# Performance work log

Measured on AMD Instinct MI355X. Metric: run time of the kernel, lower is better.

The kernel has to match this reference:

```python
import jax, jax.numpy as jnp
import numpy as np

N = 16384          # num nodes
D_IN, D_HID, D_OUT = 512, 256, 64
S = 4096           # sampled nodes per layer


def setup_inputs() -> dict:
    key = jax.random.key(0)
    ks = jax.random.split(key, 8)
    X = jax.random.normal(ks[0], (N, D_IN), dtype=jnp.float32)
    A_hat = jax.random.uniform(ks[1], (N, N), dtype=jnp.float32)
    W1 = jax.random.normal(ks[2], (D_IN, D_HID), dtype=jnp.float32) * 0.05
    b1 = jax.random.normal(ks[3], (D_HID,), dtype=jnp.float32) * 0.05
    W2 = jax.random.normal(ks[4], (D_HID, D_OUT), dtype=jnp.float32) * 0.05
    b2 = jax.random.normal(ks[5], (D_OUT,), dtype=jnp.float32) * 0.05
    # unique sampled node ids per layer (avoids nondeterministic duplicate scatter)
    sampled_l0 = jax.random.permutation(ks[6], N)[:S].astype(jnp.int32)
    sampled_l1 = jax.random.permutation(ks[7], N)[:S].astype(jnp.int32)
    return {"X": X, "A_hat": A_hat, "W1": W1, "b1": b1, "W2": W2, "b2": b2,
            "sampled_l0": sampled_l0, "sampled_l1": sampled_l1}


def reference(X, A_hat, W1, b1, W2, b2, sampled_l0, sampled_l1):
    n = X.shape[0]
    s0 = sampled_l0.shape[0]
    s1 = sampled_l1.shape[0]

    # ---- layer 0: sampled = l0, next_sampled = l1 ----
    H_l = jax.nn.relu(X[sampled_l0] @ W1 + b1)                 # [S, D_HID]
    # weights[i,j] = A_hat[next[i], sampled[j]] * N / S  (sampling_probs=None path)
    w0 = A_hat[sampled_l1][:, sampled_l0] * (n / s0)           # [S, S]
    agg0 = w0 @ H_l                                            # [S, D_HID]
    H = jnp.zeros((n, W1.shape[1]), dtype=X.dtype).at[sampled_l1].set(agg0)
    H = jax.nn.relu(H)                                         # inter-layer relu

    # ---- layer 1 (last): sampled = l1, next_sampled = arange(N) ----
    H_l2 = jax.nn.relu(H[sampled_l1] @ W2 + b2)                # [S, D_OUT]
    w1 = A_hat[:, sampled_l1] * (n / s1)                       # [N, S]
    out = w1 @ H_l2                                            # [N, D_OUT]; scatter to arange(N) == identity
    return out
```

## Files before the change

kernel.cpp:

```cpp
#include <hip/hip_runtime.h>
#include <hip/hip_bf16.h>
#include <stdint.h>

typedef __attribute__((ext_vector_type(8))) short short8;
typedef __attribute__((ext_vector_type(4))) float f32x4;

#define N_NODES 16384
#define D_IN    512
#define D_HID   256
#define D_OUT   64
#define S_SAMP  4096

__device__ __forceinline__ unsigned short f2bf(float f) {
  __hip_bfloat16 h = __float2bfloat16(f);
  union { __hip_bfloat16 h; unsigned short u; } cv; cv.h = h; return cv.u;
}

template<int BM, int BN, int BK, bool RELU_A>
__global__ __launch_bounds__(256)
void gemm_tn(const float* __restrict__ A, int lda,
             const int* __restrict__ arow,
             const unsigned short* __restrict__ Bt, int ldb,
             float* __restrict__ C, int ldc,
             int K, int kChunks, float scale)
{
  static_assert(BM == 64 && BK == 64 && (BN == 64 || BN == 256), "tile");
  const int mt  = blockIdx.x / kChunks;
  const int kc  = blockIdx.x % kChunks;
  const int kLen = K / kChunks;
  const int k0   = kc * kLen;
  const int tid  = threadIdx.x;
  const int lane = tid & 63;
  const int wid  = tid >> 6;
  const int l16  = lane & 15;
  const int lg   = lane >> 4;

  __shared__ unsigned short As[BM * BK];
  __shared__ unsigned short Bs[BN * BK];

  constexpr int WN  = (BN == 256) ? 4 : 2;
  constexpr int WM  = 4 / WN;
  constexpr int WTM = BM / WM;
  constexpr int WTN = BN / WN;
  constexpr int MF  = WTM / 16;
  constexpr int NF  = WTN / 16;
  const int wrow = wid / WN;
  const int wcol = wid % WN;

  f32x4 acc[MF][NF] = {};

  const int am   = tid >> 2;
  const int aseg = tid & 3;
  const int arowIdx = mt * BM + am;
  const size_t rowg = arow ? (size_t)arow[arowIdx] : (size_t)arowIdx;
  const float* aBase = A + rowg * (size_t)lda + k0 + aseg * 16;

  constexpr int SLABS = BN / 8;
  constexpr int SLABW = SLABS / 4;
  const int brow = lane >> 3;
  const int bcol = 8 * ((lane & 7) ^ brow);
  const unsigned short* bSrcLane = Bt + (size_t)brow * ldb + k0 + bcol;

  for (int ks = 0; ks < kLen; ks += BK) {
    __syncthreads();
    #pragma unroll
    for (int i = 0; i < SLABW; ++i) {
      const int s = wid * SLABW + i;
      __builtin_amdgcn_global_load_lds(
          (const __attribute__((address_space(1))) uint32_t*)(bSrcLane + (size_t)s * 8 * ldb + ks),
          (__attribute__((address_space(3))) uint32_t*)(&Bs[s * 512]),
          16, 0, 0);
    }
    {
      const float* ap = aBase + ks;
      f32x4 v0 = *(const f32x4*)(ap + 0);
      f32x4 v1 = *(const f32x4*)(ap + 4);
      f32x4 v2 = *(const f32x4*)(ap + 8);
      f32x4 v3 = *(const f32x4*)(ap + 12);
      if (RELU_A) {
        #pragma unroll
        for (int j = 0; j < 4; ++j) {
          v0[j] = fmaxf(v0[j], 0.f); v1[j] = fmaxf(v1[j], 0.f);
          v2[j] = fmaxf(v2[j], 0.f); v3[j] = fmaxf(v3[j], 0.f);
        }
      }
      short8 s0, s1;
      s0[0]=f2bf(v0[0]); s0[1]=f2bf(v0[1]); s0[2]=f2bf(v0[2]); s0[3]=f2bf(v0[3]);
      s0[4]=f2bf(v1[0]); s0[5]=f2bf(v1[1]); s0[6]=f2bf(v1[2]); s0[7]=f2bf(v1[3]);
      s1[0]=f2bf(v2[0]); s1[1]=f2bf(v2[1]); s1[2]=f2bf(v2[2]); s1[3]=f2bf(v2[3]);
      s1[4]=f2bf(v3[0]); s1[5]=f2bf(v3[1]); s1[6]=f2bf(v3[2]); s1[7]=f2bf(v3[3]);
      const int g0 = (aseg * 2)     ^ (am & 7);
      const int g1 = (aseg * 2 + 1) ^ (am & 7);
      *(short8*)&As[am * BK + g0 * 8] = s0;
      *(short8*)&As[am * BK + g1 * 8] = s1;
    }
    __syncthreads();
    #pragma unroll
    for (int kk = 0; kk < BK / 32; ++kk) {
      const int gk = kk * 4 + lg;
      short8 af[MF], bfr[NF];
      #pragma unroll
      for (int fm = 0; fm < MF; ++fm) {
        const int m = wrow * WTM + fm * 16 + l16;
        af[fm] = *(const short8*)&As[m * BK + ((gk ^ (m & 7)) * 8)];
      }
      #pragma unroll
      for (int fn = 0; fn < NF; ++fn) {
        const int n = wcol * WTN + fn * 16 + l16;
        bfr[fn] = *(const short8*)&Bs[n * BK + ((gk ^ (n & 7)) * 8)];
      }
      #pragma unroll
      for (int fm = 0; fm < MF; ++fm)
        #pragma unroll
        for (int fn = 0; fn < NF; ++fn)
          acc[fm][fn] = __builtin_amdgcn_mfma_f32_16x16x32_bf16(
              af[fm], bfr[fn], acc[fm][fn], 0, 0, 0);
    }
  }
  #pragma unroll
  for (int fm = 0; fm < MF; ++fm)
    #pragma unroll
    for (int fn = 0; fn < NF; ++fn)
      #pragma unroll
      for (int j = 0; j < 4; ++j) {
        const int r = mt * BM + wrow * WTM + fm * 16 + lg * 4 + j;
        const int c = wcol * WTN + fn * 16 + l16;
        atomicAdd(&C[(size_t)r * ldc + c], scale * acc[fm][fn][j]);
      }
}

__global__ void conv_w_t(const float* __restrict__ W1, const float* __restrict__ W2,
                         unsigned short* __restrict__ W1t, unsigned short* __restrict__ W2t) {
  const int idx = blockIdx.x * 256 + threadIdx.x;
  if (idx < D_IN * D_HID) {
    const int j = idx / D_IN, i = idx % D_IN;
    W1t[idx] = f2bf(W1[(size_t)i * D_HID + j]);
  }
  if (idx < D_HID * D_OUT) {
    const int j = idx / D_HID, i = idx % D_HID;
    W2t[idx] = f2bf(W2[(size_t)i * D_OUT + j]);
  }
}

__global__ void ep_scatter_t(const float* __restrict__ G, const float* __restrict__ bias,
                             const int* __restrict__ rows, unsigned short* __restrict__ BextT,
                             int ncol, int total) {
  const int idx = blockIdx.x * 256 + threadIdx.x;
  if (idx >= total) return;
  const int c = idx / S_SAMP;
  const int r = idx & (S_SAMP - 1);
  float v = G[(size_t)r * ncol + c] + bias[c];
  v = v > 0.f ? v : 0.f;
  BextT[(size_t)c * N_NODES + rows[r]] = f2bf(v);
}

extern "C" void kernel_launch(void* const* d_in, const int* in_sizes, int n_in,
                              void* d_out, int out_size, void* d_ws, size_t ws_size,
                              hipStream_t stream) {
  const float* X     = (const float*)d_in[0];
  const float* A_hat = (const float*)d_in[1];
  const float* W1    = (const float*)d_in[2];
  const float* b1    = (const float*)d_in[3];
  const float* W2    = (const float*)d_in[4];
  const float* b2    = (const float*)d_in[5];
  const int*   l0    = (const int*)d_in[6];
  const int*   l1    = (const int*)d_in[7];
  float* out = (float*)d_out;

  if (ws_size < (size_t)(20u << 20)) return;
  char* ws = (char*)d_ws;
  unsigned short* HextT = (unsigned short*)(ws);
  unsigned short* PextT = (unsigned short*)(ws + (8  << 20));
  float* G1 = (float*)(ws + (10 << 20));
  float* G2 = (float*)(ws + (14 << 20));
  float* G3 = (float*)(ws + (18 << 20));
  unsigned short* W1t = (unsigned short*)(ws + (19 << 20));
  unsigned short* W2t = (unsigned short*)(ws + (19 << 20) + (256 << 10));

  hipMemsetAsync(ws,  0, (size_t)(19u << 20), stream);
  hipMemsetAsync(out, 0, (size_t)N_NODES * D_OUT * 4, stream);

  conv_w_t<<<512, 256, 0, stream>>>(W1, W2, W1t, W2t);

  gemm_tn<64, 256, 64, false><<<(S_SAMP / 64) * 4, 256, 0, stream>>>(
      X, D_IN, l0, W1t, D_IN, G1, D_HID, D_IN, 4, 1.0f);
  ep_scatter_t<<<(S_SAMP * D_HID + 255) / 256, 256, 0, stream>>>(
      G1, b1, l0, HextT, D_HID, S_SAMP * D_HID);

  gemm_tn<64, 256, 64, false><<<(S_SAMP / 64) * 8, 256, 0, stream>>>(
      A_hat, N_NODES, l1, HextT, N_NODES, G2, D_HID, N_NODES, 8, 4.0f);

  gemm_tn<64, 64, 64, true><<<(S_SAMP / 64) * 4, 256, 0, stream>>>(
      G2, D_HID, nullptr, W2t, D_HID, G3, D_OUT, D_HID, 4, 1.0f);
  ep_scatter_t<<<(S_SAMP * D_OUT + 255) / 256, 256, 0, stream>>>(
      G3, b2, l1, PextT, D_OUT, S_SAMP * D_OUT);

  gemm_tn<64, 64, 64, false><<<(N_NODES / 64) * 8, 256, 0, stream>>>(
      A_hat, N_NODES, nullptr, PextT, N_NODES, out, D_OUT, N_NODES, 8, 4.0f);
}
```

Measured before the change: 370.3 us.

## Double-buffer LDS tiles in GEMM and retune BK and split-K counts

The GEMM kernel now keeps two LDS buffers. While the current tile is computed, the next A tile is prefetched into registers and the next B tile is issued with global_load_lds, which is meant to hide global load latency behind MFMA work. BK is made configurable (32 or 64) with matching swizzle parameters. The launches are retuned: the first two GEMMs use BK=32, the A_hat×H GEMM uses 16 K-chunks, and the final N×S GEMM uses 4. The extra buffer doubles LDS use and raises register pressure, which may reduce occupancy, and more K-chunks means more atomic traffic.

```diff
diff --git a/kernel.cpp b/kernel.cpp
--- a/kernel.cpp
+++ b/kernel.cpp
@@ -24,19 +24,27 @@
              float* __restrict__ C, int ldc,
              int K, int kChunks, float scale)
 {
-  static_assert(BM == 64 && BK == 64 && (BN == 64 || BN == 256), "tile");
+  static_assert(BM == 64 && (BK == 32 || BK == 64) && (BN == 64 || BN == 256), "tile");
+  constexpr int CH    = BK / 8;
+  constexpr int RPS   = 512 / BK;
+  constexpr int SLABS = BN / RPS;
+  constexpr int SLABW = SLABS / 4;
+  constexpr int AV    = BK / 16;
+  constexpr int AC    = BK / 32;
+
   const int mt  = blockIdx.x / kChunks;
   const int kc  = blockIdx.x % kChunks;
   const int kLen = K / kChunks;
   const int k0   = kc * kLen;
+  const int nt   = kLen / BK;
   const int tid  = threadIdx.x;
   const int lane = tid & 63;
   const int wid  = tid >> 6;
   const int l16  = lane & 15;
   const int lg   = lane >> 4;
 
-  __shared__ unsigned short As[BM * BK];
-  __shared__ unsigned short Bs[BN * BK];
+  __shared__ unsigned short As[2][BM * BK];
+  __shared__ unsigned short Bs[2][BN * BK];
 
   constexpr int WN  = (BN == 256) ? 4 : 2;
   constexpr int WM  = 4 / WN;
@@ -53,48 +61,47 @@
   const int aseg = tid & 3;
   const int arowIdx = mt * BM + am;
   const size_t rowg = arow ? (size_t)arow[arowIdx] : (size_t)arowIdx;
-  const float* aBase = A + rowg * (size_t)lda + k0 + aseg * 16;
-
-  constexpr int SLABS = BN / 8;
-  constexpr int SLABW = SLABS / 4;
-  const int brow = lane >> 3;
-  const int bcol = 8 * ((lane & 7) ^ brow);
-  const unsigned short* bSrcLane = Bt + (size_t)brow * ldb + k0 + bcol;
-
-  for (int ks = 0; ks < kLen; ks += BK) {
-    __syncthreads();
+  const float* aBase = A + rowg * (size_t)lda + k0 + aseg * (BK / 4);
+
+  const int brow = lane / CH;
+  const int bcol = 8 * ((lane % CH) ^ (brow & (CH - 1)));
+  const unsigned short* bSrc = Bt + (size_t)brow * ldb + k0 + bcol;
+
+  f32x4 av[AV];
+
+  auto loadA = [&](int ks) {
+    #pragma unroll
+    for (int i = 0; i < AV; ++i) av[i] = *(const f32x4*)(aBase + ks + 4 * i);
+  };
+  auto writeA = [&](int buf) {
+    if (RELU_A) {
+      #pragma unroll
+      for (int i = 0; i < AV; ++i)
+        #pragma unroll
+        for (int j = 0; j < 4; ++j) av[i][j] = fmaxf(av[i][j], 0.f);
+    }
+    #pragma unroll
+    for (int c = 0; c < AC; ++c) {
+      short8 s;
+      s[0]=f2bf(av[2*c][0]);   s[1]=f2bf(av[2*c][1]);
+      s[2]=f2bf(av[2*c][2]);   s[3]=f2bf(av[2*c][3]);
+      s[4]=f2bf(av[2*c+1][0]); s[5]=f2bf(av[2*c+1][1]);
+      s[6]=f2bf(av[2*c+1][2]); s[7]=f2bf(av[2*c+1][3]);
+      const int g = (aseg * AC + c) ^ (am & (CH - 1));
+      *(short8*)&As[buf][am * BK + g * 8] = s;
+    }
+  };
+  auto issueB = [&](int buf, int ks) {
     #pragma unroll
     for (int i = 0; i < SLABW; ++i) {
       const int s = wid * SLABW + i;
       __builtin_amdgcn_global_load_lds(
-          (const __attribute__((address_space(1))) uint32_t*)(bSrcLane + (size_t)s * 8 * ldb + ks),
-          (__attribute__((address_space(3))) uint32_t*)(&Bs[s * 512]),
+          (const __attribute__((address_space(1))) uint32_t*)(bSrc + (size_t)s * RPS * ldb + ks),
+          (__attribute__((address_space(3))) uint32_t*)(&Bs[buf][s * 512]),
           16, 0, 0);
     }
-    {
-      const float* ap = aBase + ks;
-      f32x4 v0 = *(const f32x4*)(ap + 0);
-      f32x4 v1 = *(const f32x4*)(ap + 4);
-      f32x4 v2 = *(const f32x4*)(ap + 8);
-      f32x4 v3 = *(const f32x4*)(ap + 12);
-      if (RELU_A) {
-        #pragma unroll
-        for (int j = 0; j < 4; ++j) {
-          v0[j] = fmaxf(v0[j], 0.f); v1[j] = fmaxf(v1[j], 0.f);
-          v2[j] = fmaxf(v2[j], 0.f); v3[j] = fmaxf(v3[j], 0.f);
-        }
-      }
-      short8 s0, s1;
-      s0[0]=f2bf(v0[0]); s0[1]=f2bf(v0[1]); s0[2]=f2bf(v0[2]); s0[3]=f2bf(v0[3]);
-      s0[4]=f2bf(v1[0]); s0[5]=f2bf(v1[1]); s0[6]=f2bf(v1[2]); s0[7]=f2bf(v1[3]);
-      s1[0]=f2bf(v2[0]); s1[1]=f2bf(v2[1]); s1[2]=f2bf(v2[2]); s1[3]=f2bf(v2[3]);
-      s1[4]=f2bf(v3[0]); s1[5]=f2bf(v3[1]); s1[6]=f2bf(v3[2]); s1[7]=f2bf(v3[3]);
-      const int g0 = (aseg * 2)     ^ (am & 7);
-      const int g1 = (aseg * 2 + 1) ^ (am & 7);
-      *(short8*)&As[am * BK + g0 * 8] = s0;
-      *(short8*)&As[am * BK + g1 * 8] = s1;
-    }
-    __syncthreads();
+  };
+  auto compute = [&](int buf) {
     #pragma unroll
     for (int kk = 0; kk < BK / 32; ++kk) {
       const int gk = kk * 4 + lg;
@@ -102,12 +109,12 @@
       #pragma unroll
       for (int fm = 0; fm < MF; ++fm) {
         const int m = wrow * WTM + fm * 16 + l16;
-        af[fm] = *(const short8*)&As[m * BK + ((gk ^ (m & 7)) * 8)];
+        af[fm] = *(const short8*)&As[buf][m * BK + ((gk ^ (m & (CH - 1))) * 8)];
       }
       #pragma unroll
       for (int fn = 0; fn < NF; ++fn) {
         const int n = wcol * WTN + fn * 16 + l16;
-        bfr[fn] = *(const short8*)&Bs[n * BK + ((gk ^ (n & 7)) * 8)];
+        bfr[fn] = *(const short8*)&Bs[buf][n * BK + ((gk ^ (n & (CH - 1))) * 8)];
       }
       #pragma unroll
       for (int fm = 0; fm < MF; ++fm)
@@ -116,7 +123,26 @@
           acc[fm][fn] = __builtin_amdgcn_mfma_f32_16x16x32_bf16(
               af[fm], bfr[fn], acc[fm][fn], 0, 0, 0);
     }
+  };
+
+  loadA(0);
+  issueB(0, 0);
+  writeA(0);
+  __syncthreads();
+
+  int cur = 0;
+  for (int t = 0; t < nt; ++t) {
+    const bool more = (t + 1 < nt);
+    if (more) {
+      loadA((t + 1) * BK);
+      issueB(cur ^ 1, (t + 1) * BK);
+    }
+    compute(cur);
+    if (more) writeA(cur ^ 1);
+    __syncthreads();
+    cur ^= 1;
   }
+
   #pragma unroll
   for (int fm = 0; fm < MF; ++fm)
     #pragma unroll
@@ -182,19 +208,19 @@
 
   conv_w_t<<<512, 256, 0, stream>>>(W1, W2, W1t, W2t);
 
-  gemm_tn<64, 256, 64, false><<<(S_SAMP / 64) * 4, 256, 0, stream>>>(
+  gemm_tn<64, 256, 32, false><<<(S_SAMP / 64) * 4, 256, 0, stream>>>(
       X, D_IN, l0, W1t, D_IN, G1, D_HID, D_IN, 4, 1.0f);
   ep_scatter_t<<<(S_SAMP * D_HID + 255) / 256, 256, 0, stream>>>(
       G1, b1, l0, HextT, D_HID, S_SAMP * D_HID);
 
-  gemm_tn<64, 256, 64, false><<<(S_SAMP / 64) * 8, 256, 0, stream>>>(
-      A_hat, N_NODES, l1, HextT, N_NODES, G2, D_HID, N_NODES, 8, 4.0f);
+  gemm_tn<64, 256, 32, false><<<(S_SAMP / 64) * 16, 256, 0, stream>>>(
+      A_hat, N_NODES, l1, HextT, N_NODES, G2, D_HID, N_NODES, 16, 4.0f);
 
   gemm_tn<64, 64, 64, true><<<(S_SAMP / 64) * 4, 256, 0, stream>>>(
       G2, D_HID, nullptr, W2t, D_HID, G3, D_OUT, D_HID, 4, 1.0f);
   ep_scatter_t<<<(S_SAMP * D_OUT + 255) / 256, 256, 0, stream>>>(
       G3, b2, l1, PextT, D_OUT, S_SAMP * D_OUT);
 
-  gemm_tn<64, 64, 64, false><<<(N_NODES / 64) * 8, 256, 0, stream>>>(
-      A_hat, N_NODES, nullptr, PextT, N_NODES, out, D_OUT, N_NODES, 8, 4.0f);
-}
+  gemm_tn<64, 64, 64, false><<<(N_NODES / 64) * 4, 256, 0, stream>>>(
+      A_hat, N_NODES, nullptr, PextT, N_NODES, out, D_OUT, N_NODES, 4, 4.0f);
+}
```

Result: slower. 423.9 us (+14.5%).

## Add double-buffered streaming GEMM for final aggregation and split K further

Applied to the files above, without the earlier changes.

Adds a gemm_stream kernel for the large A_hat @ P aggregation. It loads A rows straight into registers in MFMA fragment layout, skipping the LDS staging of A, and double-buffers the B tiles via global_load_lds with explicit waitcnt and barriers, so the next tile's loads overlap the current MFMAs. The first two GEMMs also double their K-split counts for more blocks, which adds atomic traffic on the output. The B-load indexing in gemm_tn is generalised, and a min-waves launch bound targets higher occupancy.

```diff
diff --git a/kernel.cpp b/kernel.cpp
--- a/kernel.cpp
+++ b/kernel.cpp
@@ -25,6 +25,11 @@
              int K, int kChunks, float scale)
 {
   static_assert(BM == 64 && BK == 64 && (BN == 64 || BN == 256), "tile");
+  constexpr int CH    = BK / 8;
+  constexpr int RPS   = 512 / BK;
+  constexpr int SLABS = BN / RPS;
+  constexpr int SLABW = SLABS / 4;
+
   const int mt  = blockIdx.x / kChunks;
   const int kc  = blockIdx.x % kChunks;
   const int kLen = K / kChunks;
@@ -55,11 +60,9 @@
   const size_t rowg = arow ? (size_t)arow[arowIdx] : (size_t)arowIdx;
   const float* aBase = A + rowg * (size_t)lda + k0 + aseg * 16;
 
-  constexpr int SLABS = BN / 8;
-  constexpr int SLABW = SLABS / 4;
-  const int brow = lane >> 3;
-  const int bcol = 8 * ((lane & 7) ^ brow);
-  const unsigned short* bSrcLane = Bt + (size_t)brow * ldb + k0 + bcol;
+  const int brow = lane / CH;
+  const int bcol = 8 * ((lane % CH) ^ (brow & (CH - 1)));
+  const unsigned short* bSrc = Bt + (size_t)brow * ldb + k0 + bcol;
 
   for (int ks = 0; ks < kLen; ks += BK) {
     __syncthreads();
@@ -67,7 +70,7 @@
     for (int i = 0; i < SLABW; ++i) {
       const int s = wid * SLABW + i;
       __builtin_amdgcn_global_load_lds(
-          (const __attribute__((address_space(1))) uint32_t*)(bSrcLane + (size_t)s * 8 * ldb + ks),
+          (const __attribute__((address_space(1))) uint32_t*)(bSrc + (size_t)s * RPS * ldb + ks),
           (__attribute__((address_space(3))) uint32_t*)(&Bs[s * 512]),
           16, 0, 0);
     }
@@ -129,6 +132,113 @@
       }
 }
 
+template<int MINW>
+__global__ __launch_bounds__(256, MINW)
+void gemm_stream(const float* __restrict__ A, int lda,
+                 const unsigned short* __restrict__ Bt, int ldb,
+                 float* __restrict__ C, int ldc,
+                 int K, int kChunks, float scale)
+{
+  constexpr int BN = 64, BK = 64;
+  constexpr int NF = BN / 16;
+  constexpr int CH = BK / 8;
+  constexpr int RPS = 512 / BK;
+  constexpr int SLABW = (BN / RPS) / 4;
+
+  const int mt   = blockIdx.x / kChunks;
+  const int kc   = blockIdx.x % kChunks;
+  const int kLen = K / kChunks;
+  const int k0   = kc * kLen;
+  const int nt   = kLen / BK;
+  const int tid  = threadIdx.x;
+  const int lane = tid & 63;
+  const int wid  = tid >> 6;
+  const int l16  = lane & 15;
+  const int lg   = lane >> 4;
+
+  __shared__ unsigned short Bs[2][BN * BK];
+
+  const int r = mt * 64 + wid * 16 + l16;
+  const float* aPtr = A + (size_t)r * lda + k0 + lg * 8;
+
+  const int brow = lane / CH;
+  const int bcol = 8 * ((lane % CH) ^ (brow & (CH - 1)));
+  const unsigned short* bSrc = Bt + (size_t)brow * ldb + k0 + bcol;
+
+  f32x4 acc[NF] = {};
+  f32x4 av[4];
+  short8 af0, af1;
+
+  auto issueB = [&](int buf, int t) {
+    #pragma unroll
+    for (int i = 0; i < SLABW; ++i) {
+      const int s = wid * SLABW + i;
+      __builtin_amdgcn_global_load_lds(
+          (const __attribute__((address_space(1))) uint32_t*)(bSrc + (size_t)s * RPS * ldb + t * BK),
+          (__attribute__((address_space(3))) uint32_t*)(&Bs[buf][s * 512]),
+          16, 0, 0);
+    }
+  };
+  auto loadA = [&](int t) {
+    #pragma unroll
+    for (int kk = 0; kk < 2; ++kk) {
+      av[2 * kk]     = *(const f32x4*)(aPtr + t * BK + kk * 32);
+      av[2 * kk + 1] = *(const f32x4*)(aPtr + t * BK + kk * 32 + 4);
+    }
+  };
+  auto cvtA = [&]() {
+    af0[0]=f2bf(av[0][0]); af0[1]=f2bf(av[0][1]); af0[2]=f2bf(av[0][2]); af0[3]=f2bf(av[0][3]);
+    af0[4]=f2bf(av[1][0]); af0[5]=f2bf(av[1][1]); af0[6]=f2bf(av[1][2]); af0[7]=f2bf(av[1][3]);
+    af1[0]=f2bf(av[2][0]); af1[1]=f2bf(av[2][1]); af1[2]=f2bf(av[2][2]); af1[3]=f2bf(av[2][3]);
+    af1[4]=f2bf(av[3][0]); af1[5]=f2bf(av[3][1]); af1[6]=f2bf(av[3][2]); af1[7]=f2bf(av[3][3]);
+  };
+  auto mfmaStep = [&](int buf) {
+    #pragma unroll
+    for (int kk = 0; kk < 2; ++kk) {
+      const short8 afk = kk ? af1 : af0;
+      #pragma unroll
+      for (int fn = 0; fn < NF; ++fn) {
+        const int n = fn * 16 + l16;
+        short8 b = *(const short8*)&Bs[buf][n * BK + (((kk * 4 + lg) ^ (n & (CH - 1))) * 8)];
+        acc[fn] = __builtin_amdgcn_mfma_f32_16x16x32_bf16(afk, b, acc[fn], 0, 0, 0);
+      }
+    }
+  };
+
+  issueB(0, 0);
+  __builtin_amdgcn_sched_barrier(0);
+  loadA(0);
+  asm volatile("s_waitcnt vmcnt(4)" ::: "memory");
+  __builtin_amdgcn_s_barrier();
+  __builtin_amdgcn_sched_barrier(0);
+
+  int buf = 0;
+  for (int t = 0; t < nt; ++t) {
+    cvtA();
+    if (t + 1 < nt) {
+      issueB(buf ^ 1, t + 1);
+      __builtin_amdgcn_sched_barrier(0);
+      loadA(t + 1);
+    }
+    mfmaStep(buf);
+    if (t + 1 < nt) {
+      asm volatile("s_waitcnt vmcnt(4)" ::: "memory");
+      __builtin_amdgcn_s_barrier();
+      __builtin_amdgcn_sched_barrier(0);
+    }
+    buf ^= 1;
+  }
+
+  #pragma unroll
+  for (int fn = 0; fn < NF; ++fn)
+    #pragma unroll
+    for (int j = 0; j < 4; ++j) {
+      const int rr = mt * 64 + wid * 16 + lg * 4 + j;
+      const int cc = fn * 16 + l16;
+      atomicAdd(&C[(size_t)rr * ldc + cc], scale * acc[fn][j]);
+    }
+}
+
 __global__ void conv_w_t(const float* __restrict__ W1, const float* __restrict__ W2,
                          unsigned short* __restrict__ W1t, unsigned short* __restrict__ W2t) {
   const int idx = blockIdx.x * 256 + threadIdx.x;
@@ -182,19 +292,19 @@
 
   conv_w_t<<<512, 256, 0, stream>>>(W1, W2, W1t, W2t);
 
-  gemm_tn<64, 256, 64, false><<<(S_SAMP / 64) * 4, 256, 0, stream>>>(
-      X, D_IN, l0, W1t, D_IN, G1, D_HID, D_IN, 4, 1.0f);
+  gemm_tn<64, 256, 64, false><<<(S_SAMP / 64) * 8, 256, 0, stream>>>(
+      X, D_IN, l0, W1t, D_IN, G1, D_HID, D_IN, 8, 1.0f);
   ep_scatter_t<<<(S_SAMP * D_HID + 255) / 256, 256, 0, stream>>>(
       G1, b1, l0, HextT, D_HID, S_SAMP * D_HID);
 
-  gemm_tn<64, 256, 64, false><<<(S_SAMP / 64) * 8, 256, 0, stream>>>(
-      A_hat, N_NODES, l1, HextT, N_NODES, G2, D_HID, N_NODES, 8, 4.0f);
+  gemm_tn<64, 256, 64, false><<<(S_SAMP / 64) * 16, 256, 0, stream>>>(
+      A_hat, N_NODES, l1, HextT, N_NODES, G2, D_HID, N_NODES, 16, 4.0f);
 
   gemm_tn<64, 64, 64, true><<<(S_SAMP / 64) * 4, 256, 0, stream>>>(
       G2, D_HID, nullptr, W2t, D_HID, G3, D_OUT, D_HID, 4, 1.0f);
   ep_scatter_t<<<(S_SAMP * D_OUT + 255) / 256, 256, 0, stream>>>(
       G3, b2, l1, PextT, D_OUT, S_SAMP * D_OUT);
 
-  gemm_tn<64, 64, 64, false><<<(N_NODES / 64) * 8, 256, 0, stream>>>(
-      A_hat, N_NODES, nullptr, PextT, N_NODES, out, D_OUT, N_NODES, 8, 4.0f);
-}
+  gemm_stream<6><<<(N_NODES / 64) * 8, 256, 0, stream>>>(
+      A_hat, N_NODES, PextT, N_NODES, out, D_OUT, N_NODES, 8, 4.0f);
+}
```

Result: slower. 411.7 us (+11.2%).
